# Performance work log

Hardware: AMD Instinct MI355X
Metric: run time of the kernel (lower is better)

The kernel has to match this reference:

```python
import jax, jax.numpy as jnp
import numpy as np

B = 2048      # query positions
N_OBS = 2048  # observed star positions
P = 15        # poly features = (d_max+1)(d_max+2)/2, d_max=4
G = 21        # graph features
E = 64        # n_graph_elems (columns of graph_dic)
D = 256       # opd_dim


def setup_inputs() -> dict:
    key = jax.random.key(0)
    k1, k2, k3, k4, k5, k6 = jax.random.split(key, 6)
    positions = jax.random.uniform(k1, (B, 2), dtype=jnp.float32)
    obs_pos = jax.random.uniform(k2, (N_OBS, 2), dtype=jnp.float32)
    poly_dic = jax.random.normal(k3, (N_OBS, P), dtype=jnp.float32)
    graph_dic = jax.random.normal(k4, (N_OBS, E), dtype=jnp.float32)
    alpha_poly = jnp.eye(P, dtype=jnp.float32)
    alpha_graph = jnp.eye(E, G, dtype=jnp.float32)
    S_poly = jax.random.uniform(k5, (P, D, D), minval=-0.001, maxval=0.001, dtype=jnp.float32)
    S_graph = jax.random.uniform(k6, (G, D, D), minval=-0.001, maxval=0.001, dtype=jnp.float32)
    return {"positions": positions, "obs_pos": obs_pos, "poly_dic": poly_dic,
            "graph_dic": graph_dic, "alpha_poly": alpha_poly, "alpha_graph": alpha_graph,
            "S_poly": S_poly, "S_graph": S_graph}


def reference(positions, obs_pos, poly_dic, graph_dic, alpha_poly, alpha_graph, S_poly, S_graph):
    # Brute-force 1-NN: [B, N_obs] squared distances, argmin over obs axis.
    d2 = jnp.sum((positions[:, None, :] - obs_pos[None, :, :]) ** 2, axis=-1)
    indices = jnp.argmin(d2, axis=1)                    # [B] int
    # Gather dictionary rows, mix with small alpha matrices.
    a_poly = poly_dic[indices] @ alpha_poly             # [B, P]
    a_graph = graph_dic[indices] @ alpha_graph          # [B, G]
    # Small-rank expansion into dense OPD maps.
    opd = (jnp.einsum('bp,pij->bij', a_poly, S_poly)
           + jnp.einsum('bg,gij->bij', a_graph, S_graph))  # [B, D, D]
    return opd
```

## Files before the change

### kernel.cpp

```cpp
#include <hip/hip_runtime.h>

#define NB 2048
#define NOBS 2048
#define NP 15
#define NG 21
#define NE 64
#define ND 256
#define NK 36
#define NDD (ND*ND)
#define RB 16
#define CT 4
#define QB 8

typedef float vfloat4 __attribute__((ext_vector_type(4)));

__global__ __launch_bounds__(256) void knn_coeff_kernel(
    const float* __restrict__ positions,
    const float* __restrict__ obs_pos,
    const float* __restrict__ poly_dic,
    const float* __restrict__ graph_dic,
    const float* __restrict__ alpha_poly,
    const float* __restrict__ alpha_graph,
    float* __restrict__ coeffT)
{
    __shared__ float2 sobs[NOBS];
    __shared__ float  sap[NP*NP];
    __shared__ float  sag[NE*NG];
    __shared__ int    sbest[QB];

    const int tid = threadIdx.x;

    const float2* obs2 = (const float2*)obs_pos;
    for (int i = tid; i < NOBS; i += 256) sobs[i] = obs2[i];
    for (int i = tid; i < NP*NP; i += 256) sap[i] = alpha_poly[i];
    for (int i = tid; i < NE*NG; i += 256) sag[i] = alpha_graph[i];
    __syncthreads();

    const int w    = tid >> 6;
    const int lane = tid & 63;
    const int half = lane >> 5;
    const int l32  = lane & 31;
    const int q    = blockIdx.x * QB + 2*w + half;

    const float qx = positions[2*q + 0];
    const float qy = positions[2*q + 1];

    unsigned long long best = ~0ull;
    #pragma unroll 8
    for (int it = 0; it < NOBS/32; ++it) {
        const int i = l32 + it*32;
        const float dx = qx - sobs[i].x;
        const float dy = qy - sobs[i].y;
        const float d2 = dx*dx + dy*dy;
        const unsigned long long key =
            ((unsigned long long)__float_as_uint(d2) << 32) | (unsigned)i;
        if (key < best) best = key;
    }
    #pragma unroll
    for (int m = 16; m > 0; m >>= 1) {
        const unsigned long long o = __shfl_xor(best, m, 32);
        if (o < best) best = o;
    }
    if (l32 == 0) sbest[2*w + half] = (int)(best & 0xffffffffu);
    __syncthreads();

    for (int t = tid; t < QB*NK; t += 256) {
        const int qq  = t / NK;
        const int k   = t - qq*NK;
        const int idx = sbest[qq];
        const int b   = blockIdx.x * QB + qq;
        float acc = 0.f;
        if (k < NP) {
            #pragma unroll
            for (int p = 0; p < NP; ++p)
                acc += poly_dic[idx*NP + p] * sap[p*NP + k];
        } else {
            const int g = k - NP;
            #pragma unroll
            for (int e = 0; e < NE; ++e)
                acc += graph_dic[idx*NE + e] * sag[e*NG + g];
        }
        coeffT[(size_t)k*NB + b] = acc;
    }
}

__global__ __launch_bounds__(256) void expand_kernel(
    const float* __restrict__ coeffT,
    const float* __restrict__ S_poly,
    const float* __restrict__ S_graph,
    float* __restrict__ out)
{
    const int j  = (blockIdx.x * 256 + threadIdx.x) * CT;
    const int b0 = blockIdx.y * RB;

    const float* __restrict__ sp = S_poly  + j;
    const float* __restrict__ sg = S_graph + j;
    const float* __restrict__ cb = coeffT + b0;

    vfloat4 acc[RB];
    #pragma unroll
    for (int r = 0; r < RB; ++r) acc[r] = (vfloat4)0.f;

    vfloat4 sv = *(const vfloat4*)sp;
    #pragma unroll
    for (int k = 0; k < NK; ++k) {
        vfloat4 svn = sv;
        if (k + 1 < NK) {
            const float* nsrc = (k + 1 < NP)
                ? (sp + (size_t)(k + 1) * NDD)
                : (sg + (size_t)(k + 1 - NP) * NDD);
            svn = *(const vfloat4*)nsrc;
        }
        const float* cr = cb + (size_t)k * NB;
        vfloat4 c0 = *(const vfloat4*)(cr + 0);
        vfloat4 c1 = *(const vfloat4*)(cr + 4);
        vfloat4 c2 = *(const vfloat4*)(cr + 8);
        vfloat4 c3 = *(const vfloat4*)(cr + 12);
        #pragma unroll
        for (int r = 0; r < 4; ++r) acc[r     ] += c0[r] * sv;
        #pragma unroll
        for (int r = 0; r < 4; ++r) acc[r + 4 ] += c1[r] * sv;
        #pragma unroll
        for (int r = 0; r < 4; ++r) acc[r + 8 ] += c2[r] * sv;
        #pragma unroll
        for (int r = 0; r < 4; ++r) acc[r + 12] += c3[r] * sv;
        sv = svn;
    }

    #pragma unroll
    for (int r = 0; r < RB; ++r) {
        __builtin_nontemporal_store(
            acc[r], (vfloat4*)(out + (size_t)(b0 + r)*NDD + j));
    }
}

extern "C" void kernel_launch(void* const* d_in, const int* in_sizes, int n_in,
                              void* d_out, int out_size, void* d_ws, size_t ws_size,
                              hipStream_t stream) {
    const float* positions   = (const float*)d_in[0];
    const float* obs_pos     = (const float*)d_in[1];
    const float* poly_dic    = (const float*)d_in[2];
    const float* graph_dic   = (const float*)d_in[3];
    const float* alpha_poly  = (const float*)d_in[4];
    const float* alpha_graph = (const float*)d_in[5];
    const float* S_poly      = (const float*)d_in[6];
    const float* S_graph     = (const float*)d_in[7];
    float* out = (float*)d_out;

    float* coeffT = (float*)d_ws;

    knn_coeff_kernel<<<NB/QB, 256, 0, stream>>>(
        positions, obs_pos, poly_dic, graph_dic, alpha_poly, alpha_graph, coeffT);

    dim3 grid2(NDD/(256*CT), NB/RB);
    expand_kernel<<<grid2, 256, 0, stream>>>(coeffT, S_poly, S_graph, out);
}
```

Before: 575.3 us.

## Keep S basis in registers and loop over multiple batch tiles per block

The expand kernel now loads all 36 basis values for its column pair into registers once, then iterates over 8 row tiles of the batch, reusing them. This removes repeated re-reads of S_poly/S_graph for every row block. In exchange, each thread covers 2 columns instead of 4, uses narrower stores, needs more registers, and the grid has fewer blocks.

```diff
diff --git a/kernel.cpp b/kernel.cpp
--- a/kernel.cpp
+++ b/kernel.cpp
@@ -9,10 +9,12 @@
 #define NK 36
 #define NDD (ND*ND)
 #define RB 16
-#define CT 4
+#define CT 2
+#define TILES 8
 #define QB 8
 
 typedef float vfloat4 __attribute__((ext_vector_type(4)));
+typedef float vfloat2 __attribute__((ext_vector_type(2)));
 
 __global__ __launch_bounds__(256) void knn_coeff_kernel(
     const float* __restrict__ positions,
@@ -91,46 +93,47 @@
     float* __restrict__ out)
 {
     const int j  = (blockIdx.x * 256 + threadIdx.x) * CT;
-    const int b0 = blockIdx.y * RB;
+    const int y0 = blockIdx.y * TILES;
 
-    const float* __restrict__ sp = S_poly  + j;
-    const float* __restrict__ sg = S_graph + j;
-    const float* __restrict__ cb = coeffT + b0;
+    vfloat2 sreg[NK];
+    #pragma unroll
+    for (int k = 0; k < NP; ++k)
+        sreg[k] = *(const vfloat2*)(S_poly + (size_t)k*NDD + j);
+    #pragma unroll
+    for (int k = 0; k < NG; ++k)
+        sreg[NP + k] = *(const vfloat2*)(S_graph + (size_t)k*NDD + j);
 
-    vfloat4 acc[RB];
-    #pragma unroll
-    for (int r = 0; r < RB; ++r) acc[r] = (vfloat4)0.f;
+    for (int t = 0; t < TILES; ++t) {
+        const int b0 = (y0 + t) * RB;
+        const float* __restrict__ cb = coeffT + b0;
 
-    vfloat4 sv = *(const vfloat4*)sp;
-    #pragma unroll
-    for (int k = 0; k < NK; ++k) {
-        vfloat4 svn = sv;
-        if (k + 1 < NK) {
-            const float* nsrc = (k + 1 < NP)
-                ? (sp + (size_t)(k + 1) * NDD)
-                : (sg + (size_t)(k + 1 - NP) * NDD);
-            svn = *(const vfloat4*)nsrc;
+        vfloat2 acc[RB];
+        #pragma unroll
+        for (int r = 0; r < RB; ++r) acc[r] = (vfloat2)0.f;
+
+        #pragma unroll
+        for (int k = 0; k < NK; ++k) {
+            const float* cr = cb + (size_t)k * NB;
+            vfloat4 c0 = *(const vfloat4*)(cr + 0);
+            vfloat4 c1 = *(const vfloat4*)(cr + 4);
+            vfloat4 c2 = *(const vfloat4*)(cr + 8);
+            vfloat4 c3 = *(const vfloat4*)(cr + 12);
+            const vfloat2 sv = sreg[k];
+            #pragma unroll
+            for (int r = 0; r < 4; ++r) acc[r     ] += c0[r] * sv;
+            #pragma unroll
+            for (int r = 0; r < 4; ++r) acc[r + 4 ] += c1[r] * sv;
+            #pragma unroll
+            for (int r = 0; r < 4; ++r) acc[r + 8 ] += c2[r] * sv;
+            #pragma unroll
+            for (int r = 0; r < 4; ++r) acc[r + 12] += c3[r] * sv;
         }
-        const float* cr = cb + (size_t)k * NB;
-        vfloat4 c0 = *(const vfloat4*)(cr + 0);
-        vfloat4 c1 = *(const vfloat4*)(cr + 4);
-        vfloat4 c2 = *(const vfloat4*)(cr + 8);
-        vfloat4 c3 = *(const vfloat4*)(cr + 12);
+
         #pragma unroll
-        for (int r = 0; r < 4; ++r) acc[r     ] += c0[r] * sv;
-        #pragma unroll
-        for (int r = 0; r < 4; ++r) acc[r + 4 ] += c1[r] * sv;
-        #pragma unroll
-        for (int r = 0; r < 4; ++r) acc[r + 8 ] += c2[r] * sv;
-        #pragma unroll
-        for (int r = 0; r < 4; ++r) acc[r + 12] += c3[r] * sv;
-        sv = svn;
-    }
-
-    #pragma unroll
-    for (int r = 0; r < RB; ++r) {
-        __builtin_nontemporal_store(
-            acc[r], (vfloat4*)(out + (size_t)(b0 + r)*NDD + j));
+        for (int r = 0; r < RB; ++r) {
+            __builtin_nontemporal_store(
+                acc[r], (vfloat2*)(out + (size_t)(b0 + r)*NDD + j));
+        }
     }
 }
 
@@ -152,6 +155,6 @@
     knn_coeff_kernel<<<NB/QB, 256, 0, stream>>>(
         positions, obs_pos, poly_dic, graph_dic, alpha_poly, alpha_graph, coeffT);
 
-    dim3 grid2(NDD/(256*CT), NB/RB);
+    dim3 grid2(NDD/(256*CT), (NB/RB)/TILES);
     expand_kernel<<<grid2, 256, 0, stream>>>(coeffT, S_poly, S_graph, out);
 }
```

Measured after the change: 628.0 us. +9.2%, slower.
